# Kernel optimization log

Measured on AMD Instinct MI355X. Metric: run time of the kernel, lower is better.

The kernel has to match this reference:

```python
import jax, jax.numpy as jnp
import numpy as np

NUM_LAYERS = 12
D = 256          # d_model
H = 8            # n_head
DK = D // H      # qk_dim = v_dim = 32
FFD = 1024       # ffd_dim
B, L = 32, 448
EPS = 1e-6
MAXLEN = 500


def _sinusoidal_pos_emb(maxlen, hidden_dim):
    depth = hidden_dim / 2
    positions = np.arange(maxlen, dtype=np.float32)[:, None]
    depths = np.arange(depth, dtype=np.float32)[None, :] / depth
    angle_rads = positions * (1.0 / np.power(10000.0, depths))
    pe = np.concatenate([np.sin(angle_rads), np.cos(angle_rads)], axis=-1)
    return jnp.asarray(pe, jnp.float32)


def setup_inputs() -> dict:
    key = jax.random.key(0)
    ks = jax.random.split(key, 16)
    s = 0.02
    inp = {
        "x": jax.random.normal(ks[0], (B, L, D), jnp.float32),
        "mask": jnp.zeros((B, L), jnp.bool_),
        "pos_emb": _sinusoidal_pos_emb(MAXLEN - 1, D)[:L],  # [L, D]
        "Wq": jax.random.normal(ks[1], (NUM_LAYERS, D, D), jnp.float32) * s,
        "bq": jnp.zeros((NUM_LAYERS, D), jnp.float32),
        "Wk": jax.random.normal(ks[2], (NUM_LAYERS, D, D), jnp.float32) * s,
        "bk": jnp.zeros((NUM_LAYERS, D), jnp.float32),
        "Wv": jax.random.normal(ks[3], (NUM_LAYERS, D, D), jnp.float32) * s,
        "bv": jnp.zeros((NUM_LAYERS, D), jnp.float32),
        "Wo": jax.random.normal(ks[4], (NUM_LAYERS, D, D), jnp.float32) * s,
        "bo": jnp.zeros((NUM_LAYERS, D), jnp.float32),
        "W1": jax.random.normal(ks[5], (NUM_LAYERS, D, FFD), jnp.float32) * s,
        "bf1": jnp.zeros((NUM_LAYERS, FFD), jnp.float32),
        "W2": jax.random.normal(ks[6], (NUM_LAYERS, FFD, D), jnp.float32) * s,
        "bf2": jnp.zeros((NUM_LAYERS, D), jnp.float32),
        "ln1_g": jnp.ones((NUM_LAYERS, D), jnp.float32),
        "ln1_b": jnp.zeros((NUM_LAYERS, D), jnp.float32),
        "ln2_g": jnp.ones((NUM_LAYERS, D), jnp.float32),
        "ln2_b": jnp.zeros((NUM_LAYERS, D), jnp.float32),
    }
    return inp


def _layer_norm(x, g, b):
    mu = jnp.mean(x, axis=-1, keepdims=True)
    var = jnp.mean(jnp.square(x - mu), axis=-1, keepdims=True)
    return (x - mu) * jax.lax.rsqrt(var + EPS) * g + b


def _encoder_forward(x, mask, pos_emb, Wq, bq, Wk, bk, Wv, bv, Wo, bo,
                     W1, bf1, W2, bf2, ln1_g, ln1_b, ln2_g, ln2_b):
    Bx, Lx, _ = x.shape
    scale = 1.0 / np.sqrt(DK)
    x = x + pos_emb[None, :Lx, :]
    mask_b = mask[:, None, None, :]  # [B,1,1,L], True = masked
    for i in range(NUM_LAYERS):
        # --- pre-norm attention ---
        nx = _layer_norm(x, ln1_g[i], ln1_b[i])
        q = (nx @ Wq[i] + bq[i]).reshape(Bx, Lx, H, DK)
        k = (nx @ Wk[i] + bk[i]).reshape(Bx, Lx, H, DK)
        v = (nx @ Wv[i] + bv[i]).reshape(Bx, Lx, H, DK)
        dot = jnp.einsum("bihd,bjhd->bhij", q, k) * scale
        dot = jnp.where(mask_b, -10000.0, dot)
        attn = jax.nn.softmax(dot, axis=-1)
        o = jnp.einsum("bhij,bjhd->bihd", attn, v).reshape(Bx, Lx, D)
        x = x + (o @ Wo[i] + bo[i])
        # --- pre-norm FFN (exact GELU, as torch nn.GELU) ---
        nx2 = _layer_norm(x, ln2_g[i], ln2_b[i])
        h = jax.nn.gelu(nx2 @ W1[i] + bf1[i], approximate=False)
        x = x + (h @ W2[i] + bf2[i])
    return x


def reference(x, mask, pos_emb, Wq, bq, Wk, bk, Wv, bv, Wo, bo,
              W1, bf1, W2, bf2, ln1_g, ln1_b, ln2_g, ln2_b):
    return _encoder_forward(x, mask, pos_emb, Wq, bq, Wk, bk, Wv, bv, Wo, bo,
                            W1, bf1, W2, bf2, ln1_g, ln1_b, ln2_g, ln2_b)
```

## Files before the change

kernel.cpp:

```cpp
#include <hip/hip_runtime.h>

#define NL 12
#define DM 256
#define FFDIM 1024
#define BBATCH 32
#define LSEQ 448
#define MTOK (BBATCH*LSEQ)
#define EPSF 1e-6f
#define QSCALE_LOG2E (0.17677669529663687f * 1.4426950408889634f)

typedef __attribute__((ext_vector_type(8))) short bf16x8;
typedef __attribute__((ext_vector_type(4))) float f32x4;
typedef unsigned short u16;
typedef unsigned int u32;

__device__ __forceinline__ u16 f2bf(float f) {
    union { float f; u32 u; } v; v.f = f;
    u32 r = v.u + 0x7fffu + ((v.u >> 16) & 1u);
    return (u16)(r >> 16);
}
__device__ __forceinline__ float gelu_exact(float x) {
    return 0.5f * x * (1.0f + erff(x * 0.70710678118654752f));
}
__device__ __forceinline__ void gload16(const u16* g, u16* l) {
    __builtin_amdgcn_global_load_lds(
        (const __attribute__((address_space(1))) u32*)g,
        (__attribute__((address_space(3))) u32*)l, 16, 0, 0);
}

__global__ __launch_bounds__(256) void add_pos_k(
    const float* __restrict__ x, const float* __restrict__ pe, float* __restrict__ out)
{
    int i = blockIdx.x * 256 + threadIdx.x;
    float4 xv = ((const float4*)x)[i];
    float4 pv = ((const float4*)pe)[i % (LSEQ * DM / 4)];
    float4 r;
    r.x = xv.x + pv.x; r.y = xv.y + pv.y; r.z = xv.z + pv.z; r.w = xv.w + pv.w;
    ((float4*)out)[i] = r;
}

__global__ __launch_bounds__(256) void ln_k(
    const float* __restrict__ x, const float* __restrict__ g,
    const float* __restrict__ b, u16* __restrict__ out)
{
    const int w = threadIdx.x >> 6, lane = threadIdx.x & 63;
    const int row = blockIdx.x * 4 + w;
    float4 v = ((const float4*)(x + (size_t)row * DM))[lane];
    float s = v.x + v.y + v.z + v.w;
#pragma unroll
    for (int off = 32; off; off >>= 1) s += __shfl_xor(s, off);
    float mu = s * (1.0f / 256.0f);
    float d0 = v.x - mu, d1 = v.y - mu, d2 = v.z - mu, d3 = v.w - mu;
    float sq = d0*d0 + d1*d1 + d2*d2 + d3*d3;
#pragma unroll
    for (int off = 32; off; off >>= 1) sq += __shfl_xor(sq, off);
    float rs = rsqrtf(sq * (1.0f / 256.0f) + EPSF);
    float4 gv = ((const float4*)g)[lane];
    float4 bv = ((const float4*)b)[lane];
    ushort4 o;
    o.x = f2bf(d0 * rs * gv.x + bv.x);
    o.y = f2bf(d1 * rs * gv.y + bv.y);
    o.z = f2bf(d2 * rs * gv.z + bv.z);
    o.w = f2bf(d3 * rs * gv.w + bv.w);
    *(ushort4*)(out + (size_t)row * DM + lane * 4) = o;
}

__global__ __launch_bounds__(256) void twt_k(
    const float* __restrict__ in, u16* __restrict__ out,
    int K, int N, int in_lstride, int out_lstride)
{
    __shared__ float tl[32][33];
    const int l = blockIdx.z;
    const int n0 = blockIdx.x * 32, k0 = blockIdx.y * 32;
    const int tx = threadIdx.x & 31, ty = threadIdx.x >> 5;
    const float* src = in + (size_t)l * in_lstride;
#pragma unroll
    for (int i = 0; i < 4; ++i)
        tl[ty + 8*i][tx] = src[(size_t)(k0 + ty + 8*i) * N + n0 + tx];
    __syncthreads();
    u16* dst = out + (size_t)l * out_lstride;
#pragma unroll
    for (int i = 0; i < 4; ++i)
        dst[(size_t)(n0 + ty + 8*i) * K + k0 + tx] = f2bf(tl[tx][ty + 8*i]);
}

__global__ __launch_bounds__(256) void pack_bias_k(
    const float* __restrict__ bq, const float* __restrict__ bk,
    const float* __restrict__ bv, float* __restrict__ bqkv)
{
    int i = blockIdx.x * 256 + threadIdx.x;
    if (i >= NL * 768) return;
    int l = i / 768, c = i % 768;
    float v = (c < 256) ? bq[l*256 + c] : (c < 512) ? bk[l*256 + c - 256] : bv[l*256 + c - 512];
    bqkv[i] = v;
}

template<int BM, int BN, int EPI>
__global__ __launch_bounds__(256, (BN == 64) ? 4 : 3) void mm_k(
    const u16* __restrict__ A, int lda, const u16* __restrict__ Bt,
    const float* __restrict__ bias, void* __restrict__ C, int ldc, int K,
    u16* __restrict__ vtg)
{
    __shared__ u16 As[2 * BM * 32];
    __shared__ u16 Bs[2 * BN * 32];
    constexpr int MT = (BM * BN) / 4096;
    constexpr int APANEL = BM * 32;
    constexpr int BPANEL = BN * 32;
    const int tid = threadIdx.x;
    const int by = blockIdx.x, bx = blockIdx.y;
    const int w = tid >> 6, lane = tid & 63;
    const int lm = lane & 15, lk = lane >> 4;
    const int m0 = (BN == 128) ? ((w >> 1) * 64) : (w * (MT * 16));
    const int n0 = (BN == 128) ? ((w & 1) * 64) : 0;
    const int lrow = lane >> 2, lcol = (lane & 3) * 8;

    const u16* Ab = A + (size_t)(by * BM) * lda;
    const u16* Bb = Bt + (size_t)(bx * BN) * K;

    f32x4 zz = {0.f, 0.f, 0.f, 0.f};
    f32x4 acc[MT][4];
#pragma unroll
    for (int i = 0; i < MT; ++i)
#pragma unroll
        for (int j = 0; j < 4; ++j) acc[i][j] = zz;

    for (int k0 = 0; k0 < K; k0 += 64) {
        __syncthreads();
#pragma unroll
        for (int p = 0; p < 2; ++p) {
            if constexpr (BM == 128) {
#pragma unroll
                for (int i = 0; i < 2; ++i) {
                    int seg = w * 2 + i;
                    gload16(Ab + (size_t)(seg * 16 + lrow) * lda + k0 + p * 32 + lcol,
                            &As[p * APANEL + seg * 512]);
                }
            } else {
                gload16(Ab + (size_t)(w * 16 + lrow) * lda + k0 + p * 32 + lcol,
                        &As[p * APANEL + w * 512]);
            }
            if constexpr (BN == 128) {
#pragma unroll
                for (int i = 0; i < 2; ++i) {
                    int seg = w * 2 + i;
                    gload16(Bb + (size_t)(seg * 16 + lrow) * K + k0 + p * 32 + lcol,
                            &Bs[p * BPANEL + seg * 512]);
                }
            } else {
                gload16(Bb + (size_t)(w * 16 + lrow) * K + k0 + p * 32 + lcol,
                        &Bs[p * BPANEL + w * 512]);
            }
        }
        __syncthreads();

#pragma unroll
        for (int p = 0; p < 2; ++p) {
            bf16x8 af[MT], bfr[4];
#pragma unroll
            for (int mt = 0; mt < MT; ++mt)
                af[mt] = *(const bf16x8*)&As[p * APANEL + (m0 + mt*16 + lm)*32 + lk*8];
#pragma unroll
            for (int nt = 0; nt < 4; ++nt)
                bfr[nt] = *(const bf16x8*)&Bs[p * BPANEL + (n0 + nt*16 + lm)*32 + lk*8];
#pragma unroll
            for (int mt = 0; mt < MT; ++mt)
#pragma unroll
                for (int nt = 0; nt < 4; ++nt)
                    acc[mt][nt] = __builtin_amdgcn_mfma_f32_16x16x32_bf16(af[mt], bfr[nt], acc[mt][nt], 0, 0, 0);
        }
    }

    float bv[4];
#pragma unroll
    for (int nt = 0; nt < 4; ++nt) bv[nt] = bias[bx*BN + n0 + nt*16 + lm];
#pragma unroll
    for (int mt = 0; mt < MT; ++mt) {
#pragma unroll
        for (int r = 0; r < 4; ++r) {
            int grow = by*BM + m0 + mt*16 + lk*4 + r;
            u32 bidx = 0; int srow = 0;
            if constexpr (EPI == 3) {
                bidx = (u32)grow / 448u;
                srow = grow - (int)bidx * 448;
            }
#pragma unroll
            for (int nt = 0; nt < 4; ++nt) {
                int gcol = bx*BN + n0 + nt*16 + lm;
                float vv = acc[mt][nt][r] + bv[nt];
                if constexpr (EPI == 0) {
                    ((u16*)C)[(size_t)grow * ldc + gcol] = f2bf(vv);
                } else if constexpr (EPI == 1) {
                    ((u16*)C)[(size_t)grow * ldc + gcol] = f2bf(gelu_exact(vv));
                } else if constexpr (EPI == 3) {
                    if (gcol < 256) {
                        ((u16*)C)[(size_t)grow * ldc + gcol] = f2bf(vv * QSCALE_LOG2E);
                    } else if (gcol < 512) {
                        ((u16*)C)[(size_t)grow * ldc + gcol] = f2bf(vv);
                    } else {
                        int c = gcol - 512;
                        int h = c >> 5, d = c & 31;
                        vtg[((size_t)(bidx*8 + h)*32 + d)*448 + srow] = f2bf(vv);
                    }
                } else {
                    float* p = (float*)C + (size_t)grow * ldc + gcol;
                    *p += vv;
                }
            }
        }
    }
}

__global__ __launch_bounds__(256, 4) void attn_k(
    const u16* __restrict__ qkv, const u16* __restrict__ vtg,
    const unsigned char* __restrict__ mask, u16* __restrict__ ob)
{
    __shared__ u16 Klds[448 * 32];
    __shared__ u16 Plds[4][16 * 68];
    const int tid = threadIdx.x, w = tid >> 6, lane = tid & 63;
    const int lm = lane & 15, lk = lane >> 4;
    const int bid = blockIdx.x;
    const int bh = bid & 255, sg = bid >> 8;
    const int b = bh >> 3, h = bh & 7;
    const size_t rowbase = (size_t)b * LSEQ;

#pragma unroll
    for (int i = 0; i < 7; ++i) {
        int seg = w * 7 + i;
        gload16(qkv + (rowbase + seg * 16 + (lane >> 2)) * 768 + 256 + h * 32 + (lane & 3) * 8,
                &Klds[seg * 512]);
    }
    unsigned mbits = 0;
#pragma unroll
    for (int t = 0; t < 28; ++t)
        mbits |= (mask[b * LSEQ + t * 16 + lm] ? 1u : 0u) << t;
    __syncthreads();

    const u16* Vb = vtg + (size_t)bh * 32 * 448;
    f32x4 zz = {0.f, 0.f, 0.f, 0.f};

    const int q0 = (sg * 4 + w) * 16;
    bf16x8 qf = *(const bf16x8*)(qkv + (rowbase + q0 + lm) * 768 + h * 32 + lk * 8);

    f32x4 oacc[2] = {zz, zz};
    float sum[4] = {0.f, 0.f, 0.f, 0.f};
    u16* P = &Plds[w][0];
#pragma unroll
    for (int cc = 0; cc < 7; ++cc) {
#pragma unroll
        for (int tt = 0; tt < 4; ++tt) {
            int t = cc*4 + tt;
            bf16x8 kf = *(const bf16x8*)&Klds[(t*16 + lm)*32 + lk*8];
            f32x4 s = __builtin_amdgcn_mfma_f32_16x16x32_bf16(qf, kf, zz, 0, 0, 0);
            bool m = (mbits >> t) & 1;
#pragma unroll
            for (int r = 0; r < 4; ++r) {
                float e = m ? 0.f : exp2f(s[r]);
                sum[r] += e;
                P[(lk*4 + r)*68 + tt*16 + lm] = f2bf(e);
            }
        }
        bf16x8 pa0 = *(const bf16x8*)&P[lm*68 + lk*8];
        bf16x8 pa1 = *(const bf16x8*)&P[lm*68 + 32 + lk*8];
#pragma unroll
        for (int dt = 0; dt < 2; ++dt) {
            bf16x8 vb0 = *(const bf16x8*)(Vb + (size_t)(dt*16 + lm)*448 + cc*64 + lk*8);
            bf16x8 vb1 = *(const bf16x8*)(Vb + (size_t)(dt*16 + lm)*448 + cc*64 + 32 + lk*8);
            oacc[dt] = __builtin_amdgcn_mfma_f32_16x16x32_bf16(pa0, vb0, oacc[dt], 0, 0, 0);
            oacc[dt] = __builtin_amdgcn_mfma_f32_16x16x32_bf16(pa1, vb1, oacc[dt], 0, 0, 0);
        }
    }
#pragma unroll
    for (int off = 1; off < 16; off <<= 1)
#pragma unroll
        for (int r = 0; r < 4; ++r) sum[r] += __shfl_xor(sum[r], off);
    float inv[4];
#pragma unroll
    for (int r = 0; r < 4; ++r) inv[r] = 1.0f / sum[r];

#pragma unroll
    for (int dt = 0; dt < 2; ++dt)
#pragma unroll
        for (int r = 0; r < 4; ++r)
            ob[(rowbase + q0 + lk*4 + r)*256 + h*32 + dt*16 + lm] = f2bf(oacc[dt][r] * inv[r]);
}

extern "C" void kernel_launch(void* const* d_in, const int* in_sizes, int n_in,
                              void* d_out, int out_size, void* d_ws, size_t ws_size,
                              hipStream_t stream)
{
    const float* x_in = (const float*)d_in[0];
    const unsigned char* mask = (const unsigned char*)d_in[1];
    const float* pe   = (const float*)d_in[2];
    const float* Wq = (const float*)d_in[3];
    const float* bq = (const float*)d_in[4];
    const float* Wk = (const float*)d_in[5];
    const float* bk = (const float*)d_in[6];
    const float* Wv = (const float*)d_in[7];
    const float* bv = (const float*)d_in[8];
    const float* Wo = (const float*)d_in[9];
    const float* bo = (const float*)d_in[10];
    const float* W1 = (const float*)d_in[11];
    const float* bf1 = (const float*)d_in[12];
    const float* W2 = (const float*)d_in[13];
    const float* bf2 = (const float*)d_in[14];
    const float* ln1_g = (const float*)d_in[15];
    const float* ln1_b = (const float*)d_in[16];
    const float* ln2_g = (const float*)d_in[17];
    const float* ln2_b = (const float*)d_in[18];

    float* x = (float*)d_out;
    u16* ws = (u16*)d_ws;
    u16* nx   = ws;
    u16* qkv  = nx + 3670016;
    u16* ob   = qkv + 11010048;
    u16* vtg  = ob + 3670016;
    u16* hb   = qkv;
    u16* wqkvt = vtg + 3670016;
    u16* wot  = wqkvt + 2359296;
    u16* w1t  = wot + 786432;
    u16* w2t  = w1t + 3145728;
    float* bqkv = (float*)(w2t + 3145728);

    add_pos_k<<<MTOK * DM / 1024, 256, 0, stream>>>(x_in, pe, x);

    twt_k<<<dim3(8, 8, NL), 256, 0, stream>>>(Wq, wqkvt,          256, 256, 65536, 196608);
    twt_k<<<dim3(8, 8, NL), 256, 0, stream>>>(Wk, wqkvt + 65536,  256, 256, 65536, 196608);
    twt_k<<<dim3(8, 8, NL), 256, 0, stream>>>(Wv, wqkvt + 131072, 256, 256, 65536, 196608);
    twt_k<<<dim3(8, 8, NL), 256, 0, stream>>>(Wo, wot, 256, 256, 65536, 65536);
    twt_k<<<dim3(32, 8, NL), 256, 0, stream>>>(W1, w1t, 256, 1024, 262144, 262144);
    twt_k<<<dim3(8, 32, NL), 256, 0, stream>>>(W2, w2t, 1024, 256, 262144, 262144);
    pack_bias_k<<<(NL * 768 + 255) / 256, 256, 0, stream>>>(bq, bk, bv, bqkv);

    for (int l = 0; l < NL; ++l) {
        ln_k<<<MTOK / 4, 256, 0, stream>>>(x, ln1_g + l*256, ln1_b + l*256, nx);
        mm_k<128, 128, 3><<<dim3(112, 6), 256, 0, stream>>>(
            nx, 256, wqkvt + (size_t)l*196608, bqkv + l*768, qkv, 768, 256, vtg);
        attn_k<<<1792, 256, 0, stream>>>(qkv, vtg, mask, ob);
        mm_k<128, 64, 2><<<dim3(112, 4), 256, 0, stream>>>(
            ob, 256, wot + (size_t)l*65536, bo + l*256, x, 256, 256, nullptr);
        ln_k<<<MTOK / 4, 256, 0, stream>>>(x, ln2_g + l*256, ln2_b + l*256, nx);
        mm_k<128, 128, 1><<<dim3(112, 8), 256, 0, stream>>>(
            nx, 256, w1t + (size_t)l*262144, bf1 + l*1024, hb, 1024, 256, nullptr);
        mm_k<128, 64, 2><<<dim3(112, 4), 256, 0, stream>>>(
            hb, 1024, w2t + (size_t)l*262144, bf2 + l*256, x, 256, 1024, nullptr);
    }
}
```

Before: 1.473 ms.

## Double-buffer GEMM K-loop with prefetch and vectorize V-transpose epilogue stores

```diff
diff --git a/kernel.cpp b/kernel.cpp
--- a/kernel.cpp
+++ b/kernel.cpp
@@ -95,26 +95,24 @@
     bqkv[i] = v;
 }
 
-template<int BM, int BN, int EPI>
+template<int BN, int EPI>
 __global__ __launch_bounds__(256, (BN == 64) ? 4 : 3) void mm_k(
     const u16* __restrict__ A, int lda, const u16* __restrict__ Bt,
     const float* __restrict__ bias, void* __restrict__ C, int ldc, int K,
     u16* __restrict__ vtg)
 {
-    __shared__ u16 As[2 * BM * 32];
-    __shared__ u16 Bs[2 * BN * 32];
-    constexpr int MT = (BM * BN) / 4096;
-    constexpr int APANEL = BM * 32;
-    constexpr int BPANEL = BN * 32;
+    __shared__ u16 As[2][128 * 32];
+    __shared__ u16 Bs[2][BN * 32];
+    constexpr int MT = BN / 32;
     const int tid = threadIdx.x;
     const int by = blockIdx.x, bx = blockIdx.y;
     const int w = tid >> 6, lane = tid & 63;
     const int lm = lane & 15, lk = lane >> 4;
-    const int m0 = (BN == 128) ? ((w >> 1) * 64) : (w * (MT * 16));
+    const int m0 = (BN == 128) ? ((w >> 1) * 64) : (w * 32);
     const int n0 = (BN == 128) ? ((w & 1) * 64) : 0;
     const int lrow = lane >> 2, lcol = (lane & 3) * 8;
 
-    const u16* Ab = A + (size_t)(by * BM) * lda;
+    const u16* Ab = A + (size_t)(by * 128) * lda;
     const u16* Bb = Bt + (size_t)(bx * BN) * K;
 
     f32x4 zz = {0.f, 0.f, 0.f, 0.f};
@@ -124,87 +122,85 @@
 #pragma unroll
         for (int j = 0; j < 4; ++j) acc[i][j] = zz;
 
-    for (int k0 = 0; k0 < K; k0 += 64) {
+    auto stage = [&](int buf, int k0) {
+#pragma unroll
+        for (int i = 0; i < 2; ++i) {
+            int seg = w * 2 + i;
+            gload16(Ab + (size_t)(seg * 16 + lrow) * lda + k0 + lcol, &As[buf][seg * 512]);
+        }
+        if constexpr (BN == 128) {
+#pragma unroll
+            for (int i = 0; i < 2; ++i) {
+                int seg = w * 2 + i;
+                gload16(Bb + (size_t)(seg * 16 + lrow) * K + k0 + lcol, &Bs[buf][seg * 512]);
+            }
+        } else {
+            gload16(Bb + (size_t)(w * 16 + lrow) * K + k0 + lcol, &Bs[buf][w * 512]);
+        }
+    };
+
+    stage(0, 0);
+    const int NK = K >> 5;
+    for (int it = 0; it < NK; ++it) {
+        const int cur = it & 1;
         __syncthreads();
-#pragma unroll
-        for (int p = 0; p < 2; ++p) {
-            if constexpr (BM == 128) {
-#pragma unroll
-                for (int i = 0; i < 2; ++i) {
-                    int seg = w * 2 + i;
-                    gload16(Ab + (size_t)(seg * 16 + lrow) * lda + k0 + p * 32 + lcol,
-                            &As[p * APANEL + seg * 512]);
+        if (it + 1 < NK) stage(1 - cur, (it + 1) * 32);
+        bf16x8 af[MT], bfr[4];
+#pragma unroll
+        for (int mt = 0; mt < MT; ++mt)
+            af[mt] = *(const bf16x8*)&As[cur][(m0 + mt*16 + lm)*32 + lk*8];
+#pragma unroll
+        for (int nt = 0; nt < 4; ++nt)
+            bfr[nt] = *(const bf16x8*)&Bs[cur][(n0 + nt*16 + lm)*32 + lk*8];
+#pragma unroll
+        for (int mt = 0; mt < MT; ++mt)
+#pragma unroll
+            for (int nt = 0; nt < 4; ++nt)
+                acc[mt][nt] = __builtin_amdgcn_mfma_f32_16x16x32_bf16(af[mt], bfr[nt], acc[mt][nt], 0, 0, 0);
+    }
+
+    float bv[4];
+#pragma unroll
+    for (int nt = 0; nt < 4; ++nt) bv[nt] = bias[bx*BN + n0 + nt*16 + lm];
+#pragma unroll
+    for (int mt = 0; mt < MT; ++mt) {
+        int grow0 = by*128 + m0 + mt*16 + lk*4;
+#pragma unroll
+        for (int nt = 0; nt < 4; ++nt) {
+            int gcol = bx*BN + n0 + nt*16 + lm;
+            float v0 = acc[mt][nt][0] + bv[nt];
+            float v1 = acc[mt][nt][1] + bv[nt];
+            float v2 = acc[mt][nt][2] + bv[nt];
+            float v3 = acc[mt][nt][3] + bv[nt];
+            if constexpr (EPI == 1) {
+                u16* cp = (u16*)C + (size_t)grow0 * ldc + gcol;
+                cp[0]            = f2bf(gelu_exact(v0));
+                cp[ldc]          = f2bf(gelu_exact(v1));
+                cp[2*(size_t)ldc] = f2bf(gelu_exact(v2));
+                cp[3*(size_t)ldc] = f2bf(gelu_exact(v3));
+            } else if constexpr (EPI == 3) {
+                if (gcol < 512) {
+                    float qs = (gcol < 256) ? QSCALE_LOG2E : 1.0f;
+                    u16* cp = (u16*)C + (size_t)grow0 * ldc + gcol;
+                    cp[0]            = f2bf(v0 * qs);
+                    cp[ldc]          = f2bf(v1 * qs);
+                    cp[2*(size_t)ldc] = f2bf(v2 * qs);
+                    cp[3*(size_t)ldc] = f2bf(v3 * qs);
+                } else {
+                    int c = gcol - 512;
+                    int hh = c >> 5, d = c & 31;
+                    u32 bidx = (u32)grow0 / 448u;
+                    int srow = grow0 - (int)bidx * 448;
+                    ushort4 st;
+                    st.x = f2bf(v0); st.y = f2bf(v1); st.z = f2bf(v2); st.w = f2bf(v3);
+                    *(ushort4*)&vtg[((size_t)(bidx*8 + hh)*32 + d)*448 + srow] = st;
                 }
             } else {
-                gload16(Ab + (size_t)(w * 16 + lrow) * lda + k0 + p * 32 + lcol,
-                        &As[p * APANEL + w * 512]);
-            }
-            if constexpr (BN == 128) {
-#pragma unroll
-                for (int i = 0; i < 2; ++i) {
-                    int seg = w * 2 + i;
-                    gload16(Bb + (size_t)(seg * 16 + lrow) * K + k0 + p * 32 + lcol,
-                            &Bs[p * BPANEL + seg * 512]);
-                }
-            } else {
-                gload16(Bb + (size_t)(w * 16 + lrow) * K + k0 + p * 32 + lcol,
-                        &Bs[p * BPANEL + w * 512]);
-            }
-        }
-        __syncthreads();
-
-#pragma unroll
-        for (int p = 0; p < 2; ++p) {
-            bf16x8 af[MT], bfr[4];
-#pragma unroll
-            for (int mt = 0; mt < MT; ++mt)
-                af[mt] = *(const bf16x8*)&As[p * APANEL + (m0 + mt*16 + lm)*32 + lk*8];
-#pragma unroll
-            for (int nt = 0; nt < 4; ++nt)
-                bfr[nt] = *(const bf16x8*)&Bs[p * BPANEL + (n0 + nt*16 + lm)*32 + lk*8];
-#pragma unroll
-            for (int mt = 0; mt < MT; ++mt)
-#pragma unroll
-                for (int nt = 0; nt < 4; ++nt)
-                    acc[mt][nt] = __builtin_amdgcn_mfma_f32_16x16x32_bf16(af[mt], bfr[nt], acc[mt][nt], 0, 0, 0);
-        }
-    }
-
-    float bv[4];
-#pragma unroll
-    for (int nt = 0; nt < 4; ++nt) bv[nt] = bias[bx*BN + n0 + nt*16 + lm];
-#pragma unroll
-    for (int mt = 0; mt < MT; ++mt) {
-#pragma unroll
-        for (int r = 0; r < 4; ++r) {
-            int grow = by*BM + m0 + mt*16 + lk*4 + r;
-            u32 bidx = 0; int srow = 0;
-            if constexpr (EPI == 3) {
-                bidx = (u32)grow / 448u;
-                srow = grow - (int)bidx * 448;
-            }
-#pragma unroll
-            for (int nt = 0; nt < 4; ++nt) {
-                int gcol = bx*BN + n0 + nt*16 + lm;
-                float vv = acc[mt][nt][r] + bv[nt];
-                if constexpr (EPI == 0) {
-                    ((u16*)C)[(size_t)grow * ldc + gcol] = f2bf(vv);
-                } else if constexpr (EPI == 1) {
-                    ((u16*)C)[(size_t)grow * ldc + gcol] = f2bf(gelu_exact(vv));
-                } else if constexpr (EPI == 3) {
-                    if (gcol < 256) {
-                        ((u16*)C)[(size_t)grow * ldc + gcol] = f2bf(vv * QSCALE_LOG2E);
-                    } else if (gcol < 512) {
-                        ((u16*)C)[(size_t)grow * ldc + gcol] = f2bf(vv);
-                    } else {
-                        int c = gcol - 512;
-                        int h = c >> 5, d = c & 31;
-                        vtg[((size_t)(bidx*8 + h)*32 + d)*448 + srow] = f2bf(vv);
-                    }
-                } else {
-                    float* p = (float*)C + (size_t)grow * ldc + gcol;
-                    *p += vv;
-                }
+                float* p = (float*)C + (size_t)grow0 * ldc + gcol;
+                p[0]   += v0;
+                p[ldc] += v1;
+                p[2*(size_t)ldc] += v2;
+                p[3*(size_t)ldc] += v3;
             }
         }
     }
@@ -333,15 +329,15 @@
 
     for (int l = 0; l < NL; ++l) {
         ln_k<<<MTOK / 4, 256, 0, stream>>>(x, ln1_g + l*256, ln1_b + l*256, nx);
-        mm_k<128, 128, 3><<<dim3(112, 6), 256, 0, stream>>>(
+        mm_k<128, 3><<<dim3(112, 6), 256, 0, stream>>>(
             nx, 256, wqkvt + (size_t)l*196608, bqkv + l*768, qkv, 768, 256, vtg);
         attn_k<<<1792, 256, 0, stream>>>(qkv, vtg, mask, ob);
-        mm_k<128, 64, 2><<<dim3(112, 4), 256, 0, stream>>>(
+        mm_k<64, 2><<<dim3(112, 4), 256, 0, stream>>>(
             ob, 256, wot + (size_t)l*65536, bo + l*256, x, 256, 256, nullptr);
         ln_k<<<MTOK / 4, 256, 0, stream>>>(x, ln2_g + l*256, ln2_b + l*256, nx);
-        mm_k<128, 128, 1><<<dim3(112, 8), 256, 0, stream>>>(
+        mm_k<128, 1><<<dim3(112, 8), 256, 0, stream>>>(
             nx, 256, w1t + (size_t)l*262144, bf1 + l*1024, hb, 1024, 256, nullptr);
-        mm_k<128, 64, 2><<<dim3(112, 4), 256, 0, stream>>>(
+        mm_k<64, 2><<<dim3(112, 4), 256, 0, stream>>>(
             hb, 1024, w2t + (size_t)l*262144, bf2 + l*256, x, 256, 1024, nullptr);
     }
 }
```

After: 1.541 ms. +4.6%, slower.
